# Optimization experiments

Measured on AMD Instinct MI355X. Metric: run time of the kernel, lower is better.

Reference implementation:

```python
import jax, jax.numpy as jnp
import numpy as np

B, N, D, H = 2, 512, 256, 256  # batch, seq_len, input_dim, hidden_dim
H2 = H // 2


def setup_inputs() -> dict:
    key = jax.random.key(0)
    ks = jax.random.split(key, 12)
    def lin(kw, kb, fan_in, fan_out):
        bound = 1.0 / np.sqrt(fan_in)
        W = jax.random.uniform(kw, (fan_in, fan_out), jnp.float32, -bound, bound)
        b = jax.random.uniform(kb, (fan_out,), jnp.float32, -bound, bound)
        return W, b
    W1, b1 = lin(ks[0], ks[1], 2 * D, H)
    W2, b2 = lin(ks[2], ks[3], H, H2)
    W3, b3 = lin(ks[4], ks[5], H2, 1)
    Wg, bg = lin(ks[6], ks[7], D, H)
    x = jax.random.normal(ks[8], (B, N, D), jnp.float32)
    base_adj = jax.random.uniform(ks[9], (B, N, N), jnp.float32)
    return {"x": x, "base_adj": base_adj, "W1": W1, "b1": b1,
            "W2": W2, "b2": b2, "W3": W3, "b3": b3, "Wg": Wg, "bg": bg}


def reference(x, base_adj, W1, b1, W2, b2, W3, b3, Wg, bg):
    # x: [B,N,D], base_adj: [B,N,N]
    Din = x.shape[-1]
    n = x.shape[1]
    # Linear on concat([x_i, x_j]) == x_i @ W1[:D] + x_j @ W1[D:]  (same math,
    # avoids materializing the [B,N,N,2D] pair tensor)
    left = jnp.einsum('bid,dh->bih', x, W1[:Din])    # [B,N,H]
    right = jnp.einsum('bjd,dh->bjh', x, W1[Din:])   # [B,N,H]
    h = jax.nn.relu(left[:, :, None, :] + right[:, None, :, :] + b1)  # [B,N,N,H]
    h = jax.nn.relu(jnp.einsum('bijh,hk->bijk', h, W2) + b2)          # [B,N,N,H/2]
    edge_weights = jax.nn.sigmoid(jnp.einsum('bijk,k->bij', h, W3[:, 0]) + b3[0])
    dynamic_adj = base_adj * edge_weights + jnp.eye(n, dtype=x.dtype)[None]
    dynamic_adj = jax.nn.softmax(dynamic_adj, axis=-1)
    agg = jnp.matmul(dynamic_adj, x)                 # [B,N,D]
    return jnp.einsum('bnd,dh->bnh', agg, Wg) + bg   # [B,N,H]
```

## Files before the change

### kernel.cpp

```cpp
#include <hip/hip_runtime.h>
#include <hip/hip_bf16.h>

#define NB 2
#define NN 512
#define ND 256
#define NH 256
#define NH2 128
#define JT 32

typedef __bf16 bf16x8 __attribute__((ext_vector_type(8)));
typedef __bf16 bf16x4 __attribute__((ext_vector_type(4)));
typedef float f32x4 __attribute__((ext_vector_type(4)));

__device__ __forceinline__ void gload_lds16(const void* g, void* l) {
  __builtin_amdgcn_global_load_lds((const __attribute__((address_space(1))) unsigned int*)g,
                                   (__attribute__((address_space(3))) unsigned int*)l, 16, 0, 0);
}
__device__ __forceinline__ float bflo(unsigned d) { return __uint_as_float(d << 16); }
__device__ __forceinline__ float bfhi(unsigned d) { return __uint_as_float(d & 0xffff0000u); }

__global__ __launch_bounds__(256) void prep_kernel(
    const float* __restrict__ x, const float* __restrict__ W1,
    const float* __restrict__ b1, const float* __restrict__ Wg,
    const float* __restrict__ bg, const float* __restrict__ W2,
    float* __restrict__ Lb, __bf16* __restrict__ Rb16,
    __bf16* __restrict__ XWt, __bf16* __restrict__ W2b) {
  const int blk = blockIdx.x;
  const int tid = threadIdx.x;
  __shared__ float xs[2][ND];
  __shared__ __align__(16) f32x4 part[4 * 384];
  const int r0 = blk * 2;
  xs[0][tid] = x[r0 * ND + tid];
  xs[1][tid] = x[(r0 + 1) * ND + tid];
  if (tid < 64) {
    const int idx = blk * 64 + tid;
    const int hh = idx >> 7, kk = idx & 127;
    W2b[kk * NH + hh] = (__bf16)W2[idx];
  }
  __syncthreads();

  const int dg = tid >> 6;
  const int hq = tid & 63;
  f32x4 acc[2][3];
  #pragma unroll
  for (int r = 0; r < 2; ++r)
    #pragma unroll
    for (int m = 0; m < 3; ++m) acc[r][m] = (f32x4){0.f, 0.f, 0.f, 0.f};

  const int d0 = dg * 64;
  #pragma unroll 4
  for (int it = 0; it < 64; ++it) {
    const int d = d0 + it;
    const f32x4 wl = *(const f32x4*)(W1 + d * NH + hq * 4);
    const f32x4 wr = *(const f32x4*)(W1 + (ND + d) * NH + hq * 4);
    const f32x4 wg = *(const f32x4*)(Wg + d * NH + hq * 4);
    const float x0 = xs[0][d], x1 = xs[1][d];
    acc[0][0] += x0 * wl;  acc[0][1] += x0 * wr;  acc[0][2] += x0 * wg;
    acc[1][0] += x1 * wl;  acc[1][1] += x1 * wr;  acc[1][2] += x1 * wg;
  }
  #pragma unroll
  for (int r = 0; r < 2; ++r)
    #pragma unroll
    for (int m = 0; m < 3; ++m)
      part[dg * 384 + (r * 3 + m) * 64 + hq] = acc[r][m];
  __syncthreads();

  for (int s = tid; s < 384; s += 256) {
    f32x4 sum = part[s] + part[384 + s] + part[768 + s] + part[1152 + s];
    const int r = s / 192;
    const int rem = s - r * 192;
    const int m = rem >> 6;
    const int h = (rem & 63) * 4;
    const int row = r0 + r;
    if (m == 0) {
      const f32x4 bv = *(const f32x4*)(b1 + h);
      *(f32x4*)(Lb + row * NH + h) = sum + bv;
    } else if (m == 1) {
      bf16x4 o;
      #pragma unroll
      for (int e = 0; e < 4; ++e) o[e] = (__bf16)sum[e];
      *(bf16x4*)(Rb16 + row * NH + h) = o;
    } else {
      const f32x4 v = sum + *(const f32x4*)(bg + h);
      const int bb = row >> 9, jj = row & (NN - 1);
      #pragma unroll
      for (int e = 0; e < 4; ++e)
        XWt[bb * (NH * NN) + (h + e) * NN + jj] = (__bf16)v[e];
    }
  }
}

__global__ __launch_bounds__(256, 4) void edge_kernel(
    const float* __restrict__ base_adj,
    const float* __restrict__ b2, const float* __restrict__ W3,
    const float* __restrict__ b3, const float* __restrict__ Lb,
    const __bf16* __restrict__ Rb16, const __bf16* __restrict__ XWt,
    const __bf16* __restrict__ W2b, float* __restrict__ out) {
  __shared__ __align__(16) __bf16 Rs[JT * NH];
  __shared__ __align__(16) __bf16 Hs[JT * NH];
  __shared__ __align__(16) float Lbs[NH];
  __shared__ __align__(16) float adjs[NN];
  __shared__ __align__(16) float ew[NN];
  __shared__ float red[4][JT];
  __shared__ float b2s[NH2], W3s[NH2];
  __shared__ float sred[8];

  const int blk = blockIdx.x;
  const int tid = threadIdx.x;
  const int lane = tid & 63;
  const int w = tid >> 6;
  const int lr = lane & 15;
  const int lg = lane >> 4;
  const int b = blk >> 9;
  const int i = blk & (NN - 1);

  const __bf16* Rbb = Rb16 + b * NN * NH;
  const __bf16* XWtb = XWt + b * NH * NN;

  {
    const int laneoff = (lane >> 5) * NH + (lane & 31) * 8;
    #pragma unroll
    for (int q = 0; q < 4; ++q) {
      const __bf16* src = Rbb + (w * 4 + q) * 2 * NH + laneoff;
      gload_lds16(src, (char*)Rs + (w * 4 + q) * 1024);
    }
  }
  bf16x8 bfr[8][2];
  #pragma unroll
  for (int ks8 = 0; ks8 < 8; ++ks8)
    #pragma unroll
    for (int kb = 0; kb < 2; ++kb)
      bfr[ks8][kb] = *(const bf16x8*)(W2b + (w * 32 + kb * 16 + lr) * NH + ks8 * 32 + lg * 8);

  Lbs[tid] = Lb[blk * NH + tid];
  adjs[tid] = base_adj[(b * NN + i) * NN + tid];
  adjs[tid + 256] = base_adj[(b * NN + i) * NN + tid + 256];
  if (tid < NH2) { b2s[tid] = b2[tid]; W3s[tid] = W3[tid]; }
  const float b3v = b3[0];
  asm volatile("s_waitcnt vmcnt(0)" ::: "memory");
  __syncthreads();

  const int cth = tid & 31;
  const int rowth = tid >> 5;
  float l8[8];
  #pragma unroll
  for (int e = 0; e < 8; ++e) l8[e] = Lbs[cth * 8 + e];
  const unsigned rsAddr0 = tid * 16;
  const unsigned hsAddr0 = rowth * 512 + ((cth ^ (rowth & 7)) << 4);

  for (int jt = 0; jt < 16; ++jt) {
    #pragma unroll
    for (int it = 0; it < 4; ++it) {
      const uint4 rv = *(const uint4*)((const char*)Rs + rsAddr0 + it * 4096);
      bf16x8 hb;
      #pragma unroll
      for (int e = 0; e < 4; ++e) {
        const unsigned d = ((const unsigned*)&rv)[e];
        float t0 = bflo(d) + l8[2 * e];
        float t1 = bfhi(d) + l8[2 * e + 1];
        t0 = t0 > 0.f ? t0 : 0.f;
        t1 = t1 > 0.f ? t1 : 0.f;
        hb[2 * e] = (__bf16)t0;
        hb[2 * e + 1] = (__bf16)t1;
      }
      *(bf16x8*)((char*)Hs + hsAddr0 + it * 4096) = hb;
    }
    __syncthreads();

    if (jt < 15) {
      const int laneoff = (lane >> 5) * NH + (lane & 31) * 8;
      const __bf16* base = Rbb + (jt + 1) * (JT * NH);
      #pragma unroll
      for (int q = 0; q < 4; ++q) {
        const __bf16* src = base + (w * 4 + q) * 2 * NH + laneoff;
        gload_lds16(src, (char*)Rs + (w * 4 + q) * 1024);
      }
    }

    f32x4 acc[2][2];
    #pragma unroll
    for (int ja = 0; ja < 2; ++ja)
      #pragma unroll
      for (int kb = 0; kb < 2; ++kb) acc[ja][kb] = (f32x4){0.f, 0.f, 0.f, 0.f};
    __builtin_amdgcn_s_setprio(1);
    #pragma unroll
    for (int ks8 = 0; ks8 < 8; ++ks8) {
      bf16x8 af[2];
      #pragma unroll
      for (int ja = 0; ja < 2; ++ja)
        af[ja] = *(const bf16x8*)((const char*)Hs + (ja * 16 + lr) * 512 + (((ks8 * 4 + lg) ^ (lr & 7)) << 4));
      #pragma unroll
      for (int ja = 0; ja < 2; ++ja)
        #pragma unroll
        for (int kb = 0; kb < 2; ++kb)
          acc[ja][kb] = __builtin_amdgcn_mfma_f32_16x16x32_bf16(af[ja], bfr[ks8][kb], acc[ja][kb], 0, 0, 0);
    }
    __builtin_amdgcn_s_setprio(0);

    #pragma unroll
    for (int ja = 0; ja < 2; ++ja) {
      #pragma unroll
      for (int r = 0; r < 4; ++r) {
        const int k0 = w * 32 + lr;
        float t0 = acc[ja][0][r] + b2s[k0];
        float t1 = acc[ja][1][r] + b2s[k0 + 16];
        t0 = t0 > 0.f ? t0 : 0.f;
        t1 = t1 > 0.f ? t1 : 0.f;
        float s = fmaf(t0, W3s[k0], t1 * W3s[k0 + 16]);
        s += __shfl_xor(s, 1, 16);
        s += __shfl_xor(s, 2, 16);
        s += __shfl_xor(s, 4, 16);
        s += __shfl_xor(s, 8, 16);
        if (lr == 0) red[w][ja * 16 + lg * 4 + r] = s;
      }
    }
    asm volatile("s_waitcnt vmcnt(0)" ::: "memory");
    __syncthreads();

    if (tid < JT) {
      const float v = red[0][tid] + red[1][tid] + red[2][tid] + red[3][tid] + b3v;
      const float sg = 1.f / (1.f + __expf(-v));
      const int j = jt * JT + tid;
      ew[j] = adjs[j] * sg + ((j == i) ? 1.f : 0.f);
    }
  }
  __syncthreads();

  float v0 = ew[tid], v1 = ew[tid + 256];
  float m = fmaxf(v0, v1);
  #pragma unroll
  for (int off = 1; off < 64; off <<= 1) m = fmaxf(m, __shfl_xor(m, off, 64));
  if (lane == 0) sred[w] = m;
  __syncthreads();
  m = fmaxf(fmaxf(sred[0], sred[1]), fmaxf(sred[2], sred[3]));
  const float e0 = __expf(v0 - m), e1 = __expf(v1 - m);
  float ssum = e0 + e1;
  #pragma unroll
  for (int off = 1; off < 64; off <<= 1) ssum += __shfl_xor(ssum, off, 64);
  if (lane == 0) sred[4 + w] = ssum;
  __syncthreads();
  const float inv = 1.f / (sred[4] + sred[5] + sred[6] + sred[7]);
  const float p0 = e0 * inv, p1 = e1 * inv;

  __bf16* ewh = (__bf16*)ew;
  __bf16* ewl = ewh + NN;
  {
    const __bf16 h0 = (__bf16)p0;
    const __bf16 h1 = (__bf16)p1;
    ewh[tid] = h0;        ewl[tid] = (__bf16)(p0 - (float)h0);
    ewh[tid + 256] = h1;  ewl[tid + 256] = (__bf16)(p1 - (float)h1);
  }
  __syncthreads();

  const char* ewb = (const char*)ew;
  const unsigned aoff = (lr == 1 ? 1024u : 0u) + lg * 16;
  const bool azero = (lr >= 2);
  f32x4 pacc[4];
  #pragma unroll
  for (int q = 0; q < 4; ++q) pacc[q] = (f32x4){0.f, 0.f, 0.f, 0.f};
  #pragma unroll
  for (int ks = 0; ks < 16; ++ks) {
    uint4 pa = *(const uint4*)(ewb + aoff + ks * 64);
    if (azero) { pa.x = 0; pa.y = 0; pa.z = 0; pa.w = 0; }
    const bf16x8 paf = __builtin_bit_cast(bf16x8, pa);
    #pragma unroll
    for (int q = 0; q < 4; ++q) {
      const int h = w * 64 + q * 16 + lr;
      const bf16x8 bv = *(const bf16x8*)(XWtb + h * NN + ks * 32 + lg * 8);
      pacc[q] = __builtin_amdgcn_mfma_f32_16x16x32_bf16(paf, bv, pacc[q], 0, 0, 0);
    }
  }
  if (lg == 0) {
    #pragma unroll
    for (int q = 0; q < 4; ++q)
      out[blk * NH + w * 64 + q * 16 + lr] = pacc[q][0] + pacc[q][1];
  }
}

extern "C" void kernel_launch(void* const* d_in, const int* in_sizes, int n_in,
                              void* d_out, int out_size, void* d_ws, size_t ws_size,
                              hipStream_t stream) {
  const float* x        = (const float*)d_in[0];
  const float* base_adj = (const float*)d_in[1];
  const float* W1       = (const float*)d_in[2];
  const float* b1       = (const float*)d_in[3];
  const float* W2       = (const float*)d_in[4];
  const float* b2       = (const float*)d_in[5];
  const float* W3       = (const float*)d_in[6];
  const float* b3       = (const float*)d_in[7];
  const float* Wg       = (const float*)d_in[8];
  const float* bg       = (const float*)d_in[9];

  float*  Lb    = (float*)d_ws;
  __bf16* Rb16  = (__bf16*)(Lb + NB * NN * NH);
  __bf16* XWt   = Rb16 + NB * NN * NH;
  __bf16* W2b   = XWt + NB * NH * NN;
  float* outp = (float*)d_out;

  prep_kernel<<<512, 256, 0, stream>>>(x, W1, b1, Wg, bg, W2, Lb, Rb16, XWt, W2b);
  edge_kernel<<<NB * NN, 256, 0, stream>>>(base_adj, b2, W3, b3, Lb, Rb16, XWt, W2b, outp);
}
```

Before: 176.7 us.

## Retile prep GEMM into 64-row register blocks and drop MFMA priority hints

The prep kernel is rebuilt so that each block stages 64 rows of x in shared memory and computes a 32-column slice of one of the three projections (left, right or gate). Each thread then accumulates a 4x2 register tile. Before, every block reread the full weight matrices for only two rows. The new tiling cuts weight traffic roughly 32-fold and drops the cross-warp partial-sum reduction. The launch shrinks from 512 to 384 blocks, and the W2 conversion moves to the first 128 blocks. Separately, the s_setprio calls around the MFMA loop in the edge kernel are removed, which may change wave scheduling in the dominant kernel.

```diff
diff --git a/kernel.cpp b/kernel.cpp
--- a/kernel.cpp
+++ b/kernel.cpp
@@ -10,6 +10,7 @@
 
 typedef __bf16 bf16x8 __attribute__((ext_vector_type(8)));
 typedef __bf16 bf16x4 __attribute__((ext_vector_type(4)));
+typedef __bf16 bf16x2 __attribute__((ext_vector_type(2)));
 typedef float f32x4 __attribute__((ext_vector_type(4)));
 
 __device__ __forceinline__ void gload_lds16(const void* g, void* l) {
@@ -25,67 +26,76 @@
     const float* __restrict__ bg, const float* __restrict__ W2,
     float* __restrict__ Lb, __bf16* __restrict__ Rb16,
     __bf16* __restrict__ XWt, __bf16* __restrict__ W2b) {
+  __shared__ __align__(16) float xs[64 * 260];
   const int blk = blockIdx.x;
   const int tid = threadIdx.x;
-  __shared__ float xs[2][ND];
-  __shared__ __align__(16) f32x4 part[4 * 384];
-  const int r0 = blk * 2;
-  xs[0][tid] = x[r0 * ND + tid];
-  xs[1][tid] = x[(r0 + 1) * ND + tid];
-  if (tid < 64) {
-    const int idx = blk * 64 + tid;
+  if (blk < 128) {
+    const int idx = blk * 256 + tid;
     const int hh = idx >> 7, kk = idx & 127;
     W2b[kk * NH + hh] = (__bf16)W2[idx];
   }
-  __syncthreads();
-
-  const int dg = tid >> 6;
-  const int hq = tid & 63;
-  f32x4 acc[2][3];
-  #pragma unroll
-  for (int r = 0; r < 2; ++r)
-    #pragma unroll
-    for (int m = 0; m < 3; ++m) acc[r][m] = (f32x4){0.f, 0.f, 0.f, 0.f};
-
-  const int d0 = dg * 64;
-  #pragma unroll 4
-  for (int it = 0; it < 64; ++it) {
-    const int d = d0 + it;
-    const f32x4 wl = *(const f32x4*)(W1 + d * NH + hq * 4);
-    const f32x4 wr = *(const f32x4*)(W1 + (ND + d) * NH + hq * 4);
-    const f32x4 wg = *(const f32x4*)(Wg + d * NH + hq * 4);
-    const float x0 = xs[0][d], x1 = xs[1][d];
-    acc[0][0] += x0 * wl;  acc[0][1] += x0 * wr;  acc[0][2] += x0 * wg;
-    acc[1][0] += x1 * wl;  acc[1][1] += x1 * wr;  acc[1][2] += x1 * wg;
-  }
-  #pragma unroll
-  for (int r = 0; r < 2; ++r)
-    #pragma unroll
-    for (int m = 0; m < 3; ++m)
-      part[dg * 384 + (r * 3 + m) * 64 + hq] = acc[r][m];
-  __syncthreads();
-
-  for (int s = tid; s < 384; s += 256) {
-    f32x4 sum = part[s] + part[384 + s] + part[768 + s] + part[1152 + s];
-    const int r = s / 192;
-    const int rem = s - r * 192;
-    const int m = rem >> 6;
-    const int h = (rem & 63) * 4;
-    const int row = r0 + r;
-    if (m == 0) {
-      const f32x4 bv = *(const f32x4*)(b1 + h);
-      *(f32x4*)(Lb + row * NH + h) = sum + bv;
-    } else if (m == 1) {
-      bf16x4 o;
-      #pragma unroll
-      for (int e = 0; e < 4; ++e) o[e] = (__bf16)sum[e];
-      *(bf16x4*)(Rb16 + row * NH + h) = o;
-    } else {
-      const f32x4 v = sum + *(const f32x4*)(bg + h);
+  const int rg = blk / 24;
+  const int cg = blk - rg * 24;
+  const int r0 = rg * 64;
+  const int m = cg >> 3;
+  const int h0 = (cg & 7) * 32;
+  const float* Wbase = (m == 2 ? Wg : W1 + (m == 1 ? 256 * NH : 0)) + h0;
+
+  #pragma unroll
+  for (int k = 0; k < 16; ++k) {
+    const int q = k * 256 + tid;
+    const int row = q >> 6, c4 = (q & 63) << 2;
+    *(f32x4*)(xs + row * 260 + c4) = *(const f32x4*)(x + (r0 + row) * ND + c4);
+  }
+  __syncthreads();
+
+  const int cs = tid & 15;
+  const int rs = tid >> 4;
+  const float* Wc = Wbase + 2 * cs;
+  float2 acc[4];
+  #pragma unroll
+  for (int mm = 0; mm < 4; ++mm) { acc[mm].x = 0.f; acc[mm].y = 0.f; }
+
+  for (int d4 = 0; d4 < 64; ++d4) {
+    f32x4 xv[4];
+    #pragma unroll
+    for (int mm = 0; mm < 4; ++mm)
+      xv[mm] = *(const f32x4*)(xs + (rs + 16 * mm) * 260 + d4 * 4);
+    #pragma unroll
+    for (int e = 0; e < 4; ++e) {
+      const float2 wv = *(const float2*)(Wc + (d4 * 4 + e) * NH);
+      #pragma unroll
+      for (int mm = 0; mm < 4; ++mm) {
+        acc[mm].x = fmaf(xv[mm][e], wv.x, acc[mm].x);
+        acc[mm].y = fmaf(xv[mm][e], wv.y, acc[mm].y);
+      }
+    }
+  }
+
+  const int h = h0 + 2 * cs;
+  if (m == 0) {
+    const float2 bv = *(const float2*)(b1 + h);
+    #pragma unroll
+    for (int mm = 0; mm < 4; ++mm) {
+      const int row = r0 + rs + 16 * mm;
+      float2 o; o.x = acc[mm].x + bv.x; o.y = acc[mm].y + bv.y;
+      *(float2*)(Lb + row * NH + h) = o;
+    }
+  } else if (m == 1) {
+    #pragma unroll
+    for (int mm = 0; mm < 4; ++mm) {
+      const int row = r0 + rs + 16 * mm;
+      bf16x2 o; o[0] = (__bf16)acc[mm].x; o[1] = (__bf16)acc[mm].y;
+      *(bf16x2*)(Rb16 + row * NH + h) = o;
+    }
+  } else {
+    const float2 bv = *(const float2*)(bg + h);
+    #pragma unroll
+    for (int mm = 0; mm < 4; ++mm) {
+      const int row = r0 + rs + 16 * mm;
       const int bb = row >> 9, jj = row & (NN - 1);
-      #pragma unroll
-      for (int e = 0; e < 4; ++e)
-        XWt[bb * (NH * NN) + (h + e) * NN + jj] = (__bf16)v[e];
+      XWt[bb * (NH * NN) + h * NN + jj] = (__bf16)(acc[mm].x + bv.x);
+      XWt[bb * (NH * NN) + (h + 1) * NN + jj] = (__bf16)(acc[mm].y + bv.y);
     }
   }
 }
@@ -182,7 +192,6 @@
     for (int ja = 0; ja < 2; ++ja)
       #pragma unroll
       for (int kb = 0; kb < 2; ++kb) acc[ja][kb] = (f32x4){0.f, 0.f, 0.f, 0.f};
-    __builtin_amdgcn_s_setprio(1);
     #pragma unroll
     for (int ks8 = 0; ks8 < 8; ++ks8) {
       bf16x8 af[2];
@@ -195,7 +204,6 @@
         for (int kb = 0; kb < 2; ++kb)
           acc[ja][kb] = __builtin_amdgcn_mfma_f32_16x16x32_bf16(af[ja], bfr[ks8][kb], acc[ja][kb], 0, 0, 0);
     }
-    __builtin_amdgcn_s_setprio(0);
 
     #pragma unroll
     for (int ja = 0; ja < 2; ++ja) {
@@ -297,6 +305,6 @@
   __bf16* W2b   = XWt + NB * NH * NN;
   float* outp = (float*)d_out;
 
-  prep_kernel<<<512, 256, 0, stream>>>(x, W1, b1, Wg, bg, W2, Lb, Rb16, XWt, W2b);
+  prep_kernel<<<384, 256, 0, stream>>>(x, W1, b1, Wg, bg, W2, Lb, Rb16, XWt, W2b);
   edge_kernel<<<NB * NN, 256, 0, stream>>>(base_adj, b2, W3, b3, Lb, Rb16, XWt, W2b, outp);
 }
```

Result: no change. 175.9 us (-0.5%).
